# Performance work log

Hardware: AMD Instinct MI355X
Metric: run time of the kernel (lower is better)

## Reference

```python
import jax, jax.numpy as jnp
import numpy as np
import math

C = 128
KSIZE = 9
PAD = KSIZE // 2


def _conv1d(v, w, b):
    # v: [B, C, K]; w: [C_out, C_in, 9]; cross-correlation, 'same' padding (matches torch Conv2d)
    y = jax.lax.conv_general_dilated(v, w, window_strides=(1,), padding=[(PAD, PAD)],
                                     dimension_numbers=("NCH", "OIH", "NCH"))
    return y + b[None, :, None]


def _sweep(x, w, b, axis, reverse):
    # Sequential SCNN sweep along `axis` (2 = rows/vertical, 3 = cols/horizontal).
    rows = jnp.moveaxis(x, axis, 0)  # [L, B, C, K]
    if reverse:
        rows = rows[::-1]

    def step(prev, row):
        new = row + jax.nn.relu(_conv1d(prev, w, b))
        return new, new

    _, rest = jax.lax.scan(step, rows[0], rows[1:])
    out = jnp.concatenate([rows[:1], rest], axis=0)
    if reverse:
        out = out[::-1]
    return jnp.moveaxis(out, 0, axis)


def setup_inputs() -> dict:
    key = jax.random.key(0)
    ks = jax.random.split(key, 9)
    B, H, W = 32, 72, 200
    bound = math.sqrt(2.0 / (C * 9 * 5))  # SCNN paper init
    x = jax.random.normal(ks[0], (B, C, H, W), dtype=jnp.float32)
    def wgt(k):
        return jax.random.uniform(k, (C, C, KSIZE), dtype=jnp.float32, minval=-bound, maxval=bound)
    def bia(k):
        return 0.01 * jax.random.normal(k, (C,), dtype=jnp.float32)
    return {
        "x": x,
        "w_d": wgt(ks[1]), "b_d": bia(ks[2]),
        "w_u": wgt(ks[3]), "b_u": bia(ks[4]),
        "w_r": wgt(ks[5]), "b_r": bia(ks[6]),
        "w_l": wgt(ks[7]), "b_l": bia(ks[8]),
    }


def reference(x, w_d, b_d, w_u, b_u, w_r, b_r, w_l, b_l):
    # Four directional sweeps: down, up, right, left (SCNN order)
    out = _sweep(x,   w_d, b_d, axis=2, reverse=False)
    out = _sweep(out, w_u, b_u, axis=2, reverse=True)
    out = _sweep(out, w_r, b_r, axis=3, reverse=False)
    out = _sweep(out, w_l, b_l, axis=3, reverse=True)
    return out
```

## Files before the change

kernel.cpp:

```cpp
#include <hip/hip_runtime.h>

#define CC  128
#define HH  72
#define WW  200
#define HW_ (HH*WW)
#define CHW (CC*HW_)

template<int L>
__global__ __launch_bounds__(256) void step_kern(
    float* __restrict__ st, const float* __restrict__ wgt,
    const float* __restrict__ bias, int r_src, int r_dst)
{
    __shared__ float lds[CC * 40];
    const int b     = blockIdx.z;
    const int lbase = blockIdx.x * 32;
    const int cbase = blockIdx.y * 64;
    const int t     = threadIdx.x;

    const float* src = st + (size_t)b * CHW + (size_t)r_src * L;
    #pragma unroll
    for (int i = 0; i < 20; i++) {
        int idx = t + i * 256;
        int ci  = idx / 40;
        int lo  = idx - ci * 40;
        int l   = lbase - 4 + lo;
        lds[idx] = (l >= 0 && l < L) ? src[(size_t)ci * HW_ + l] : 0.f;
    }
    __syncthreads();

    const int lgrp = t & 7;
    const int cgrp = t >> 3;
    const int l0   = lbase + lgrp * 4;
    const int c0   = cbase + cgrp * 2;

    float acc[2][4] = {};
    for (int ci = 0; ci < CC; ci++) {
        float p[12];
        const float* lp = &lds[ci * 40 + lgrp * 4];
        #pragma unroll
        for (int j = 0; j < 12; j++) p[j] = lp[j];
        #pragma unroll
        for (int c = 0; c < 2; c++) {
            const float* wp = wgt + ((size_t)(c0 + c) * CC + ci) * 9;
            #pragma unroll
            for (int k = 0; k < 9; k++) {
                const float wv = wp[k];
                #pragma unroll
                for (int j = 0; j < 4; j++)
                    acc[c][j] = fmaf(wv, p[j + k], acc[c][j]);
            }
        }
    }

    if (l0 < L) {
        #pragma unroll
        for (int c = 0; c < 2; c++) {
            float* po = st + (size_t)b * CHW + (size_t)(c0 + c) * HW_
                           + (size_t)r_dst * L + l0;
            float4 v = *(float4*)po;
            const float bb = bias[c0 + c];
            v.x += fmaxf(acc[c][0] + bb, 0.f);
            v.y += fmaxf(acc[c][1] + bb, 0.f);
            v.z += fmaxf(acc[c][2] + bb, 0.f);
            v.w += fmaxf(acc[c][3] + bb, 0.f);
            *(float4*)po = v;
        }
    }
}

__global__ __launch_bounds__(256) void transpose_kern(
    const float* __restrict__ in, float* __restrict__ outp, int rows, int cols)
{
    __shared__ float tile[32][33];
    const size_t plane = (size_t)rows * cols;
    const float* ip = in   + (size_t)blockIdx.z * plane;
    float*       op = outp + (size_t)blockIdx.z * plane;
    const int c0 = blockIdx.x * 32, r0 = blockIdx.y * 32;
    const int tx = threadIdx.x, ty = threadIdx.y;

    #pragma unroll
    for (int i = 0; i < 32; i += 8) {
        int r = r0 + ty + i, c = c0 + tx;
        if (r < rows && c < cols) tile[ty + i][tx] = ip[(size_t)r * cols + c];
    }
    __syncthreads();
    #pragma unroll
    for (int i = 0; i < 32; i += 8) {
        int r = c0 + ty + i, c = r0 + tx;
        if (r < cols && c < rows) op[(size_t)r * rows + c] = tile[tx][ty + i];
    }
}

__global__ __launch_bounds__(256) void stepH_kern(
    float* __restrict__ out, const float* __restrict__ wgt,
    const float* __restrict__ bias, int w_src, int w_dst)
{
    __shared__ float lds[CC * 32];
    const int b     = blockIdx.z;
    const int hbase = blockIdx.x * 24;
    const int cbase = blockIdx.y * 32;
    const int t     = threadIdx.x;

    const float* srcb = out + (size_t)b * CHW + w_src;
    for (int i = t; i < CC * 32; i += 256) {
        int ci = i >> 5;
        int ho = i & 31;
        int h  = hbase - 4 + ho;
        lds[i] = (h >= 0 && h < HH) ? srcb[(size_t)ci * HW_ + (size_t)h * WW] : 0.f;
    }
    __syncthreads();

    const int hgrp  = t & 7;
    const int cgrp  = t >> 3;
    const int h0    = hgrp * 3;
    const int c_out = cbase + cgrp;

    float acc[3] = {};
    for (int ci = 0; ci < CC; ci++) {
        float p[11];
        const float* lp = &lds[ci * 32 + h0];
        #pragma unroll
        for (int j = 0; j < 11; j++) p[j] = lp[j];
        const float* wp = wgt + ((size_t)c_out * CC + ci) * 9;
        #pragma unroll
        for (int k = 0; k < 9; k++) {
            const float wv = wp[k];
            #pragma unroll
            for (int m = 0; m < 3; m++)
                acc[m] = fmaf(wv, p[m + k], acc[m]);
        }
    }

    const float bb = bias[c_out];
    float* po = out + (size_t)b * CHW + (size_t)c_out * HW_
                    + (size_t)(hbase + h0) * WW + w_dst;
    #pragma unroll
    for (int m = 0; m < 3; m++)
        po[(size_t)m * WW] += fmaxf(acc[m] + bb, 0.f);
}

extern "C" void kernel_launch(void* const* d_in, const int* in_sizes, int n_in,
                              void* d_out, int out_size, void* d_ws, size_t ws_size,
                              hipStream_t stream)
{
    const float* x   = (const float*)d_in[0];
    const float* w_d = (const float*)d_in[1];
    const float* b_d = (const float*)d_in[2];
    const float* w_u = (const float*)d_in[3];
    const float* b_u = (const float*)d_in[4];
    const float* w_r = (const float*)d_in[5];
    const float* b_r = (const float*)d_in[6];
    const float* w_l = (const float*)d_in[7];
    const float* b_l = (const float*)d_in[8];
    float* out = (float*)d_out;
    float* ws  = (float*)d_ws;

    const size_t bytes = (size_t)32 * CHW * sizeof(float);
    hipMemcpyAsync(out, x, bytes, hipMemcpyDeviceToDevice, stream);

    const dim3 gW(7, 2, 32), blk(256);
    for (int h = 1; h < HH; h++)
        step_kern<WW><<<gW, blk, 0, stream>>>(out, w_d, b_d, h - 1, h);
    for (int h = HH - 2; h >= 0; h--)
        step_kern<WW><<<gW, blk, 0, stream>>>(out, w_u, b_u, h + 1, h);

    if (ws_size >= bytes) {
        transpose_kern<<<dim3(7, 3, 4096), dim3(32, 8), 0, stream>>>(out, ws, HH, WW);

        const dim3 gH(3, 2, 32);
        for (int w = 1; w < WW; w++)
            step_kern<HH><<<gH, blk, 0, stream>>>(ws, w_r, b_r, w - 1, w);
        for (int w = WW - 2; w >= 0; w--)
            step_kern<HH><<<gH, blk, 0, stream>>>(ws, w_l, b_l, w + 1, w);

        transpose_kern<<<dim3(3, 7, 4096), dim3(32, 8), 0, stream>>>(ws, out, WW, HH);
    } else {
        const dim3 gB(3, 4, 32);
        for (int w = 1; w < WW; w++)
            stepH_kern<<<gB, blk, 0, stream>>>(out, w_r, b_r, w - 1, w);
        for (int w = WW - 2; w >= 0; w--)
            stepH_kern<<<gB, blk, 0, stream>>>(out, w_l, b_l, w + 1, w);
    }
}
```

Before: 20.56 ms.

## Repack conv weights into coalesced float4 layout and use new step kernel

Adds a one-time repack of all four weight tensors into a [ci][3][c_out] float4 layout, so each thread's lane maps to an output channel and weight loads become coalesced vector loads instead of scattered scalar loads. A new step kernel uses 128-thread blocks with one output channel per lane and several positions per thread. It software-prefetches the next input channel's weights and LDS window into registers. This trades a larger workspace requirement and higher register pressure for less weight-load traffic and more blocks per step.

Result: slower. 25.39 ms (+23.5%).

```diff
diff --git a/kernel.cpp b/kernel.cpp
--- a/kernel.cpp
+++ b/kernel.cpp
@@ -5,6 +5,109 @@
 #define WW  200
 #define HW_ (HH*WW)
 #define CHW (CC*HW_)
+#define WREP_FLOATS (CC*CC*12)
+
+__global__ __launch_bounds__(256) void repack_kern(
+    const float* __restrict__ w0, const float* __restrict__ w1,
+    const float* __restrict__ w2, const float* __restrict__ w3,
+    float* __restrict__ outp)
+{
+    const float* src = (blockIdx.y == 0) ? w0 : (blockIdx.y == 1) ? w1
+                     : (blockIdx.y == 2) ? w2 : w3;
+    float* dst = outp + (size_t)blockIdx.y * WREP_FLOATS;
+    int idx = blockIdx.x * 256 + threadIdx.x;
+    int c  = idx >> 7;
+    int ci = idx & 127;
+    const float* wp = src + ((size_t)c * CC + ci) * 9;
+    float v[12];
+    #pragma unroll
+    for (int k = 0; k < 9; k++) v[k] = wp[k];
+    v[9] = v[10] = v[11] = 0.f;
+    float4* o = (float4*)dst;
+    #pragma unroll
+    for (int kk = 0; kk < 3; kk++)
+        o[(ci * 3 + kk) * CC + c] = make_float4(v[kk*4], v[kk*4+1], v[kk*4+2], v[kk*4+3]);
+}
+
+template<int L, int LPT>
+__global__ __launch_bounds__(128) void step2_kern(
+    float* __restrict__ st, const float* __restrict__ wq,
+    const float* __restrict__ bias, int r_src, int r_dst)
+{
+    constexpr int TL  = 4 * LPT;
+    constexpr int WIN = TL + 8;
+    __shared__ __align__(16) float lds[CC * WIN];
+    const int b     = blockIdx.z;
+    const int lbase = blockIdx.x * TL;
+    const int cbase = blockIdx.y * 32;
+    const int t     = threadIdx.x;
+
+    const float* src = st + (size_t)b * CHW + (size_t)r_src * L;
+    #pragma unroll
+    for (int i2 = 0; i2 < (CC * WIN) / 128; i2++) {
+        int i  = t + i2 * 128;
+        int ci = i / WIN;
+        int lo = i - ci * WIN;
+        int l  = lbase - 4 + lo;
+        lds[i] = (l >= 0 && l < L) ? src[(size_t)ci * HW_ + l] : 0.f;
+    }
+    __syncthreads();
+
+    const int cgrp = t & 31;
+    const int lgrp = t >> 5;
+    const int c    = cbase + cgrp;
+    const int l0   = lbase + lgrp * LPT;
+
+    const float4* wq4 = (const float4*)wq;
+    float acc[LPT] = {};
+    float p[LPT + 8];
+    float4 w0, w1, w2;
+    {
+        const float* lp = &lds[lgrp * LPT];
+        #pragma unroll
+        for (int j = 0; j < LPT + 8; j++) p[j] = lp[j];
+        w0 = wq4[0 * CC + c];
+        w1 = wq4[1 * CC + c];
+        w2 = wq4[2 * CC + c];
+    }
+
+    for (int ci = 0; ci < CC - 1; ci++) {
+        float4 nw0 = wq4[((ci + 1) * 3 + 0) * CC + c];
+        float4 nw1 = wq4[((ci + 1) * 3 + 1) * CC + c];
+        float4 nw2 = wq4[((ci + 1) * 3 + 2) * CC + c];
+        float np[LPT + 8];
+        const float* lp = &lds[(ci + 1) * WIN + lgrp * LPT];
+        #pragma unroll
+        for (int j = 0; j < LPT + 8; j++) np[j] = lp[j];
+
+        const float wk[9] = {w0.x, w0.y, w0.z, w0.w, w1.x, w1.y, w1.z, w1.w, w2.x};
+        #pragma unroll
+        for (int k = 0; k < 9; k++)
+            #pragma unroll
+            for (int j = 0; j < LPT; j++)
+                acc[j] = fmaf(wk[k], p[j + k], acc[j]);
+
+        #pragma unroll
+        for (int j = 0; j < LPT + 8; j++) p[j] = np[j];
+        w0 = nw0; w1 = nw1; w2 = nw2;
+    }
+    {
+        const float wk[9] = {w0.x, w0.y, w0.z, w0.w, w1.x, w1.y, w1.z, w1.w, w2.x};
+        #pragma unroll
+        for (int k = 0; k < 9; k++)
+            #pragma unroll
+            for (int j = 0; j < LPT; j++)
+                acc[j] = fmaf(wk[k], p[j + k], acc[j]);
+    }
+
+    if (l0 < L) {
+        const float bb = bias[c];
+        float* po = st + (size_t)b * CHW + (size_t)c * HW_ + (size_t)r_dst * L + l0;
+        #pragma unroll
+        for (int j = 0; j < LPT; j++)
+            po[j] += fmaxf(acc[j] + bb, 0.f);
+    }
+}
 
 template<int L>
 __global__ __launch_bounds__(256) void step_kern(
@@ -155,26 +258,54 @@
     float* out = (float*)d_out;
     float* ws  = (float*)d_ws;
 
-    const size_t bytes = (size_t)32 * CHW * sizeof(float);
+    const size_t bytes      = (size_t)32 * CHW * sizeof(float);
+    const size_t wrep_bytes = (size_t)4 * WREP_FLOATS * sizeof(float);
     hipMemcpyAsync(out, x, bytes, hipMemcpyDeviceToDevice, stream);
 
-    const dim3 gW(7, 2, 32), blk(256);
-    for (int h = 1; h < HH; h++)
-        step_kern<WW><<<gW, blk, 0, stream>>>(out, w_d, b_d, h - 1, h);
-    for (int h = HH - 2; h >= 0; h--)
-        step_kern<WW><<<gW, blk, 0, stream>>>(out, w_u, b_u, h + 1, h);
-
-    if (ws_size >= bytes) {
+    if (ws_size >= bytes + wrep_bytes) {
+        float* wrep = (float*)((char*)d_ws + bytes);
+        repack_kern<<<dim3(64, 4), 256, 0, stream>>>(w_d, w_u, w_r, w_l, wrep);
+        const float* q_d = wrep + 0 * (size_t)WREP_FLOATS;
+        const float* q_u = wrep + 1 * (size_t)WREP_FLOATS;
+        const float* q_r = wrep + 2 * (size_t)WREP_FLOATS;
+        const float* q_l = wrep + 3 * (size_t)WREP_FLOATS;
+
+        const dim3 blk(128);
+        const dim3 gW(7, 4, 32);
+        for (int h = 1; h < HH; h++)
+            step2_kern<WW, 8><<<gW, blk, 0, stream>>>(out, q_d, b_d, h - 1, h);
+        for (int h = HH - 2; h >= 0; h--)
+            step2_kern<WW, 8><<<gW, blk, 0, stream>>>(out, q_u, b_u, h + 1, h);
+
         transpose_kern<<<dim3(7, 3, 4096), dim3(32, 8), 0, stream>>>(out, ws, HH, WW);
 
+        const dim3 gH(3, 4, 32);
+        for (int w = 1; w < WW; w++)
+            step2_kern<HH, 6><<<gH, blk, 0, stream>>>(ws, q_r, b_r, w - 1, w);
+        for (int w = WW - 2; w >= 0; w--)
+            step2_kern<HH, 6><<<gH, blk, 0, stream>>>(ws, q_l, b_l, w + 1, w);
+
+        transpose_kern<<<dim3(3, 7, 4096), dim3(32, 8), 0, stream>>>(ws, out, WW, HH);
+    } else if (ws_size >= bytes) {
+        const dim3 gW(7, 2, 32), blk(256);
+        for (int h = 1; h < HH; h++)
+            step_kern<WW><<<gW, blk, 0, stream>>>(out, w_d, b_d, h - 1, h);
+        for (int h = HH - 2; h >= 0; h--)
+            step_kern<WW><<<gW, blk, 0, stream>>>(out, w_u, b_u, h + 1, h);
+
+        transpose_kern<<<dim3(7, 3, 4096), dim3(32, 8), 0, stream>>>(out, ws, HH, WW);
         const dim3 gH(3, 2, 32);
         for (int w = 1; w < WW; w++)
             step_kern<HH><<<gH, blk, 0, stream>>>(ws, w_r, b_r, w - 1, w);
         for (int w = WW - 2; w >= 0; w--)
             step_kern<HH><<<gH, blk, 0, stream>>>(ws, w_l, b_l, w + 1, w);
-
         transpose_kern<<<dim3(3, 7, 4096), dim3(32, 8), 0, stream>>>(ws, out, WW, HH);
     } else {
+        const dim3 gW(7, 2, 32), blk(256);
+        for (int h = 1; h < HH; h++)
+            step_kern<WW><<<gW, blk, 0, stream>>>(out, w_d, b_d, h - 1, h);
+        for (int h = HH - 2; h >= 0; h--)
+            step_kern<WW><<<gW, blk, 0, stream>>>(out, w_u, b_u, h + 1, h);
         const dim3 gB(3, 4, 32);
         for (int w = 1; w < WW; w++)
             stepH_kern<<<gB, blk, 0, stream>>>(out, w_r, b_r, w - 1, w);
```

## Fuse per-row sweep launches into persistent kernels with per-batch atomic barriers

Applied to the files above, without the earlier changes.

Replaces the ~540 per-step kernel launches with two persistent kernels, one per sweep pair. Each kernel processes every row or column of both directions in a loop and synchronises the blocks of a batch through a global atomic counter with acquire/release spin-waits. Weights are also repacked once to a 12-float stride per tap group for aligned loads. This removes launch overhead and kernel-boundary idle time. In exchange all blocks must be co-resident or the kernel deadlocks, and the spin-waiting adds global-memory polling.

Result: slower. 30.16 ms (+46.7%).

```diff
diff --git a/kernel.cpp b/kernel.cpp
--- a/kernel.cpp
+++ b/kernel.cpp
@@ -5,6 +5,136 @@
 #define WW  200
 #define HW_ (HH*WW)
 #define CHW (CC*HW_)
+#define W12_FLOATS (CC*CC*12)
+
+__device__ float g_w12[4][W12_FLOATS];
+__device__ int   g_ctr[2][32 * 32];
+
+__global__ __launch_bounds__(256) void repack_zero_kern(
+    const float* __restrict__ w0, const float* __restrict__ w1,
+    const float* __restrict__ w2, const float* __restrict__ w3)
+{
+    if (blockIdx.x == 0 && blockIdx.y == 0) {
+        for (int i = threadIdx.x; i < 2 * 32 * 32; i += 256)
+            ((int*)g_ctr)[i] = 0;
+    }
+    const float* src = (blockIdx.y == 0) ? w0 : (blockIdx.y == 1) ? w1
+                     : (blockIdx.y == 2) ? w2 : w3;
+    float* dst = g_w12[blockIdx.y];
+    int idx = blockIdx.x * 256 + threadIdx.x;
+    const float* wp = src + (size_t)idx * 9;
+    float* op = dst + (size_t)idx * 12;
+    #pragma unroll
+    for (int k = 0; k < 9; k++) op[k] = wp[k];
+    op[9] = op[10] = op[11] = 0.f;
+}
+
+template<int L, int R, int TL, int CT, int CPT, int LPT, int BPB, int CIDX>
+__global__ __launch_bounds__(256) void sweep_pair_kern(
+    float* st, const float* __restrict__ w12f, const float* __restrict__ bf,
+    const float* __restrict__ w12b, const float* __restrict__ bbi)
+{
+    constexpr int WIN = TL + 8;
+    constexpr int NG  = TL / LPT;
+    __shared__ float lds[CC * WIN];
+    const int b     = blockIdx.z;
+    const int lbase = blockIdx.x * TL;
+    const int cbase = blockIdx.y * CT;
+    const int t     = threadIdx.x;
+    const int lgrp  = t & (NG - 1);
+    const int cgrp  = t / NG;
+    const int l0g   = lgrp * LPT;
+    const int c0    = cbase + cgrp * CPT;
+    int* myctr = &g_ctr[CIDX][b * 32];
+
+    float* stb = st + (size_t)b * CHW;
+
+    for (int ph = 0; ph < 2; ph++) {
+        const float* w12  = ph ? w12b : w12f;
+        const float* bias = ph ? bbi  : bf;
+        const int tbase   = ph ? BPB * (R - 1) : 0;
+        for (int s = 1; s <= R - 1; s++) {
+            const int r_dst  = ph ? (R - 1 - s) : s;
+            const int r_src  = ph ? (R - s)     : (s - 1);
+            const int target = tbase + BPB * (s - 1);
+            if (target > 0 && t == 0) {
+                while (__hip_atomic_load(myctr, __ATOMIC_ACQUIRE,
+                                         __HIP_MEMORY_SCOPE_AGENT) < target)
+                    __builtin_amdgcn_s_sleep(2);
+            }
+            __syncthreads();
+
+            const float* src = stb + (size_t)r_src * L;
+            for (int i = t; i < CC * WIN; i += 256) {
+                int ci = i / WIN;
+                int lo = i - ci * WIN;
+                int l  = lbase - 4 + lo;
+                lds[i] = (l >= 0 && l < L) ? src[(size_t)ci * (R * L) + l] : 0.f;
+            }
+            __syncthreads();
+
+            float acc[CPT][LPT] = {};
+            for (int ci = 0; ci < CC; ci++) {
+                float p[LPT + 8];
+                const float* lp = &lds[ci * WIN + l0g];
+                #pragma unroll
+                for (int j = 0; j < LPT + 8; j++) p[j] = lp[j];
+                #pragma unroll
+                for (int c = 0; c < CPT; c++) {
+                    const float* wp = w12 + ((size_t)(c0 + c) * CC + ci) * 12;
+                    #pragma unroll
+                    for (int k = 0; k < 9; k++) {
+                        const float wv = wp[k];
+                        #pragma unroll
+                        for (int j = 0; j < LPT; j++)
+                            acc[c][j] = fmaf(wv, p[j + k], acc[c][j]);
+                    }
+                }
+            }
+
+            const int l0 = lbase + l0g;
+            if (l0 < L) {
+                #pragma unroll
+                for (int c = 0; c < CPT; c++) {
+                    float* po = stb + (size_t)(c0 + c) * (R * L)
+                                    + (size_t)r_dst * L + l0;
+                    const float bb2 = bias[c0 + c];
+                    #pragma unroll
+                    for (int j = 0; j < LPT; j++)
+                        po[j] += fmaxf(acc[c][j] + bb2, 0.f);
+                }
+            }
+
+            __syncthreads();
+            if (t == 0)
+                __hip_atomic_fetch_add(myctr, 1, __ATOMIC_RELEASE,
+                                       __HIP_MEMORY_SCOPE_AGENT);
+        }
+    }
+}
+
+__global__ __launch_bounds__(256) void transpose_kern(
+    const float* __restrict__ in, float* __restrict__ outp, int rows, int cols)
+{
+    __shared__ float tile[32][33];
+    const size_t plane = (size_t)rows * cols;
+    const float* ip = in   + (size_t)blockIdx.z * plane;
+    float*       op = outp + (size_t)blockIdx.z * plane;
+    const int c0 = blockIdx.x * 32, r0 = blockIdx.y * 32;
+    const int tx = threadIdx.x, ty = threadIdx.y;
+
+    #pragma unroll
+    for (int i = 0; i < 32; i += 8) {
+        int r = r0 + ty + i, c = c0 + tx;
+        if (r < rows && c < cols) tile[ty + i][tx] = ip[(size_t)r * cols + c];
+    }
+    __syncthreads();
+    #pragma unroll
+    for (int i = 0; i < 32; i += 8) {
+        int r = c0 + ty + i, c = r0 + tx;
+        if (r < cols && c < rows) op[(size_t)r * rows + c] = tile[tx][ty + i];
+    }
+}
 
 template<int L>
 __global__ __launch_bounds__(256) void step_kern(
@@ -65,29 +195,6 @@
             v.w += fmaxf(acc[c][3] + bb, 0.f);
             *(float4*)po = v;
         }
-    }
-}
-
-__global__ __launch_bounds__(256) void transpose_kern(
-    const float* __restrict__ in, float* __restrict__ outp, int rows, int cols)
-{
-    __shared__ float tile[32][33];
-    const size_t plane = (size_t)rows * cols;
-    const float* ip = in   + (size_t)blockIdx.z * plane;
-    float*       op = outp + (size_t)blockIdx.z * plane;
-    const int c0 = blockIdx.x * 32, r0 = blockIdx.y * 32;
-    const int tx = threadIdx.x, ty = threadIdx.y;
-
-    #pragma unroll
-    for (int i = 0; i < 32; i += 8) {
-        int r = r0 + ty + i, c = c0 + tx;
-        if (r < rows && c < cols) tile[ty + i][tx] = ip[(size_t)r * cols + c];
-    }
-    __syncthreads();
-    #pragma unroll
-    for (int i = 0; i < 32; i += 8) {
-        int r = c0 + ty + i, c = r0 + tx;
-        if (r < cols && c < rows) op[(size_t)r * rows + c] = tile[tx][ty + i];
     }
 }
 
@@ -158,23 +265,31 @@
     const size_t bytes = (size_t)32 * CHW * sizeof(float);
     hipMemcpyAsync(out, x, bytes, hipMemcpyDeviceToDevice, stream);
 
-    const dim3 gW(7, 2, 32), blk(256);
-    for (int h = 1; h < HH; h++)
-        step_kern<WW><<<gW, blk, 0, stream>>>(out, w_d, b_d, h - 1, h);
-    for (int h = HH - 2; h >= 0; h--)
-        step_kern<WW><<<gW, blk, 0, stream>>>(out, w_u, b_u, h + 1, h);
-
     if (ws_size >= bytes) {
+        repack_zero_kern<<<dim3(64, 4), 256, 0, stream>>>(w_d, w_u, w_r, w_l);
+
+        float* q = nullptr;
+        hipGetSymbolAddress((void**)&q, HIP_SYMBOL(g_w12));
+        const float* q_d = q + 0 * (size_t)W12_FLOATS;
+        const float* q_u = q + 1 * (size_t)W12_FLOATS;
+        const float* q_r = q + 2 * (size_t)W12_FLOATS;
+        const float* q_l = q + 3 * (size_t)W12_FLOATS;
+
+        sweep_pair_kern<WW, HH, 32, 64, 2, 4, 14, 0>
+            <<<dim3(7, 2, 32), 256, 0, stream>>>(out, q_d, b_d, q_u, b_u);
+
         transpose_kern<<<dim3(7, 3, 4096), dim3(32, 8), 0, stream>>>(out, ws, HH, WW);
 
-        const dim3 gH(3, 2, 32);
-        for (int w = 1; w < WW; w++)
-            step_kern<HH><<<gH, blk, 0, stream>>>(ws, w_r, b_r, w - 1, w);
-        for (int w = WW - 2; w >= 0; w--)
-            step_kern<HH><<<gH, blk, 0, stream>>>(ws, w_l, b_l, w + 1, w);
+        sweep_pair_kern<HH, WW, 24, 32, 1, 3, 12, 1>
+            <<<dim3(3, 4, 32), 256, 0, stream>>>(ws, q_r, b_r, q_l, b_l);
 
         transpose_kern<<<dim3(3, 7, 4096), dim3(32, 8), 0, stream>>>(ws, out, WW, HH);
     } else {
+        const dim3 gW(7, 2, 32), blk(256);
+        for (int h = 1; h < HH; h++)
+            step_kern<WW><<<gW, blk, 0, stream>>>(out, w_d, b_d, h - 1, h);
+        for (int h = HH - 2; h >= 0; h--)
+            step_kern<WW><<<gW, blk, 0, stream>>>(out, w_u, b_u, h + 1, h);
         const dim3 gB(3, 4, 32);
         for (int w = 1; w < WW; w++)
             stepH_kern<<<gB, blk, 0, stream>>>(out, w_r, b_r, w - 1, w);
```
